# Kernel tuning notes

Hardware: AMD Instinct MI355X
Metric: run time of the kernel (lower is better)

Reference implementation:

```python
import jax, jax.numpy as jnp
import numpy as np

N = 4096; B = 32; LATENT = 16; UNITS = 64; NNZ = 65536; K = 2; M = 2 * K + 1

def _spmm(rows, cols, vals, x):
    # sparse [N,N] @ dense [N,FB] via gather + segment_sum
    return jax.ops.segment_sum(vals[:, None] * x[cols], rows, num_segments=N)

def _gconv(y, supports, W, b):
    # y: (B, N*F) -> Chebyshev-style diffusion over each support, then dense projection
    F = y.shape[1] // N
    x0 = y.reshape(B, N, F).transpose(1, 2, 0).reshape(N, F * B)
    xs = [x0]
    for rows, cols, vals in supports:
        x1 = _spmm(rows, cols, vals, x0)
        xs.append(x1)
        xk1, xk2 = x1, x0
        for _ in range(2, K + 1):
            x2 = 2.0 * _spmm(rows, cols, vals, xk1) - xk2
            xs.append(x2)
            xk1, xk2 = x2, xk1
    # [M,N,F,B] -> [B,N,F,M] -> [B*N, F*M], matching torch permute/reshape
    x = jnp.stack(xs).reshape(M, N, F, B).transpose(3, 1, 2, 0).reshape(B * N, F * M)
    return (x @ W + b).reshape(B, N * W.shape[1])

def setup_inputs():
    key = jax.random.key(0)
    ks = jax.random.split(key, 8)
    r = jax.random.randint(ks[0], (NNZ,), 0, N)
    c = jax.random.randint(ks[1], (NNZ,), 0, N)
    v = jax.random.uniform(ks[2], (NNZ,)) + 0.1
    d_row = jax.ops.segment_sum(v, r, num_segments=N)
    d_col = jax.ops.segment_sum(v, c, num_segments=N)
    inv_row = jnp.where(d_row > 0, 1.0 / d_row, 0.0)
    inv_col = jnp.where(d_col > 0, 1.0 / d_col, 0.0)
    # support1 = (D_out^{-1} A)^T ; support2 = (D_in^{-1} A^T)^T  (COO triples)
    s1_rows, s1_cols, s1_vals = c, r, v * inv_row[r]
    s2_rows, s2_cols, s2_vals = r, c, v * inv_col[c]
    def xavier(k, shape):
        scale = np.sqrt(2.0 / (shape[0] + shape[1])).astype(np.float32)
        return jax.random.normal(k, shape, dtype=jnp.float32) * scale
    return {
        "t_local": 0,
        "y": jax.random.normal(ks[3], (B, N * LATENT), dtype=jnp.float32),
        "W_theta": xavier(ks[4], (LATENT * M, LATENT)),
        "b_lat": jnp.ones((LATENT,), jnp.float32),  # bias_start=1.0; shared (LayerParams keys biases by length)
        "W_hid": xavier(ks[5], (LATENT * M, UNITS)),
        "b_hid": jnp.zeros((UNITS,), jnp.float32),
        "W_out": xavier(ks[6], (UNITS * M, LATENT)),
        "s1_rows": s1_rows, "s1_cols": s1_cols, "s1_vals": s1_vals,
        "s2_rows": s2_rows, "s2_cols": s2_cols, "s2_vals": s2_vals,
    }

def reference(t_local, y, W_theta, b_lat, W_hid, b_hid, W_out,
              s1_rows, s1_cols, s1_vals, s2_rows, s2_cols, s2_vals):
    supports = [(s1_rows, s1_cols, s1_vals), (s2_rows, s2_cols, s2_vals)]
    theta = jax.nn.sigmoid(_gconv(y, supports, W_theta, b_lat))
    c = jnp.tanh(_gconv(y, supports, W_hid, b_hid))   # gen_layers = 1
    c = jnp.tanh(_gconv(c, supports, W_out, b_lat))   # shared bias of length latent_dim
    return -theta * c
```

## Files before the change

kernel.cpp:

```cpp
#include <hip/hip_runtime.h>
#include <stdint.h>

#define NN    4096
#define BB    32
#define NNZE  65536
#define WA    512
#define WD    512

typedef __attribute__((ext_vector_type(8))) short bf16x8;
typedef __attribute__((ext_vector_type(4))) float f32x4;

__device__ __forceinline__ float bf2f_lo(unsigned int u) {
    union { unsigned int x; float f; } c; c.x = u << 16; return c.f;
}
__device__ __forceinline__ float bf2f_hi(unsigned int u) {
    union { unsigned int x; float f; } c; c.x = u & 0xffff0000u; return c.f;
}
__device__ __forceinline__ float bf2f(unsigned int h) {
    union { unsigned int u; float f; } c; c.u = h << 16; return c.f;
}
__device__ __forceinline__ unsigned int f2bf(float f) {
    union { float ff; unsigned int u; } c; c.ff = f;
    return (c.u + 0x7fffu + ((c.u >> 16) & 1u)) >> 16;
}

__global__ void hist2_kernel(const int* __restrict__ r1, const int* __restrict__ r2,
                             int* __restrict__ cnt1, int* __restrict__ cnt2) {
    int e = blockIdx.x * blockDim.x + threadIdx.x;
    if (e < NNZE) atomicAdd(&cnt1[r1[e]], 1);
    else          atomicAdd(&cnt2[r2[e - NNZE]], 1);
}

__global__ void scan2_kernel(int* cur1, int* rp1, int* cur2, int* rp2) {
    int* cur = (blockIdx.x == 0) ? cur1 : cur2;
    int* rp  = (blockIdx.x == 0) ? rp1  : rp2;
    __shared__ int part[256];
    int t = threadIdx.x;
    int base = t * 16;
    int loc[16];
    int s = 0;
#pragma unroll
    for (int i = 0; i < 16; ++i) { loc[i] = s; s += cur[base + i]; }
    part[t] = s;
    __syncthreads();
    for (int off = 1; off < 256; off <<= 1) {
        int v = 0;
        if (t >= off) v = part[t - off];
        __syncthreads();
        part[t] += v;
        __syncthreads();
    }
    int excl = (t == 0) ? 0 : part[t - 1];
#pragma unroll
    for (int i = 0; i < 16; ++i) rp[base + i] = excl + loc[i];
    __syncthreads();
#pragma unroll
    for (int i = 0; i < 16; ++i) cur[base + i] = rp[base + i];
    if (t == 255) rp[4096] = part[255];
}

__global__ void scatter2_kernel(const int* __restrict__ r1, const int* __restrict__ c1, const float* __restrict__ v1,
                                const int* __restrict__ r2, const int* __restrict__ c2, const float* __restrict__ v2,
                                int* __restrict__ cur1, int* __restrict__ cur2,
                                int2* __restrict__ ep1, int2* __restrict__ ep2) {
    int e = blockIdx.x * blockDim.x + threadIdx.x;
    if (e < NNZE) {
        int pos = atomicAdd(&cur1[r1[e]], 1);
        ep1[pos] = make_int2(c1[e], __float_as_int(v1[e]));
    } else {
        int ee = e - NNZE;
        int pos = atomicAdd(&cur2[r2[ee]], 1);
        ep2[pos] = make_int2(c2[ee], __float_as_int(v2[ee]));
    }
}

__global__ void transA_kernel(const float* __restrict__ y, unsigned short* __restrict__ x0h) {
    int t = threadIdx.x, n = blockIdx.x;
    int b = t & 31, q = t >> 5;
    float4 y4 = *(const float4*)(y + (size_t)b * (NN * 16) + n * 16 + 4 * q);
    uint2 o;
    o.x = f2bf(y4.x) | (f2bf(y4.y) << 16);
    o.y = f2bf(y4.z) | (f2bf(y4.w) << 16);
    *(uint2*)(x0h + (size_t)n * WA + b * 16 + 4 * q) = o;
}

struct SpmmDesc {
    const unsigned short* in;
    const unsigned short* prev;
    float* outF;
    unsigned short* outH;
    const int* rp; const int2* ep;
    float alpha, beta;
};

__device__ __forceinline__ void gather_row_lds(const unsigned short* __restrict__ in,
                                               const int* __restrict__ rp, const int2* __restrict__ ep,
                                               int row, int t, int* scol, float* sval, float* acc) {
    int beg = rp[row], end = rp[row + 1];
    for (int i0 = beg; i0 < end; i0 += 64) {
        int nn = end - i0; if (nn > 64) nn = 64;
        __syncthreads();
        if (t < nn) { int2 e = ep[i0 + t]; scol[t] = e.x; sval[t] = __int_as_float(e.y); }
        __syncthreads();
#pragma unroll 4
        for (int j = 0; j < nn; ++j) {
            const uint4* xr = (const uint4*)(in + (size_t)scol[j] * WD);
            uint4 xv = xr[t];
            float v = sval[j];
            acc[0] += v * bf2f_lo(xv.x); acc[1] += v * bf2f_hi(xv.x);
            acc[2] += v * bf2f_lo(xv.y); acc[3] += v * bf2f_hi(xv.y);
            acc[4] += v * bf2f_lo(xv.z); acc[5] += v * bf2f_hi(xv.z);
            acc[6] += v * bf2f_lo(xv.w); acc[7] += v * bf2f_hi(xv.w);
        }
    }
}

__launch_bounds__(64)
__global__ void spmmD_kernel(SpmmDesc q0, SpmmDesc q1, SpmmDesc q2, SpmmDesc q3, int ninst) {
    __shared__ int scol[64];
    __shared__ float sval[64];
    int blk = blockIdx.x;
    int xcd = blk & 7;
    int idx = blk >> 3;
    int spx = 8 / ninst;
    int inst = xcd / spx;
    int sub  = xcd - inst * spx;
    int row  = sub * (NN / spx) + idx;
    SpmmDesc q = (inst == 0) ? q0 : (inst == 1) ? q1 : (inst == 2) ? q2 : q3;
    int t = threadIdx.x;
    float acc[8];
#pragma unroll
    for (int k = 0; k < 8; ++k) acc[k] = 0.f;
    gather_row_lds(q.in, q.rp, q.ep, row, t, scol, sval, acc);
    float r[8];
#pragma unroll
    for (int k = 0; k < 8; ++k) r[k] = q.alpha * acc[k];
    if (q.prev) {
        uint4 pv = ((const uint4*)(q.prev + (size_t)row * WD))[t];
        r[0] += q.beta * bf2f_lo(pv.x); r[1] += q.beta * bf2f_hi(pv.x);
        r[2] += q.beta * bf2f_lo(pv.y); r[3] += q.beta * bf2f_hi(pv.y);
        r[4] += q.beta * bf2f_lo(pv.z); r[5] += q.beta * bf2f_hi(pv.z);
        r[6] += q.beta * bf2f_lo(pv.w); r[7] += q.beta * bf2f_hi(pv.w);
    }
    if (q.outF) {
        float* po = q.outF + (size_t)row * WD + t * 8;
        *(float4*)(po)     = make_float4(r[0], r[1], r[2], r[3]);
        *(float4*)(po + 4) = make_float4(r[4], r[5], r[6], r[7]);
    } else {
        uint4 o;
        o.x = f2bf(r[0]) | (f2bf(r[1]) << 16);
        o.y = f2bf(r[2]) | (f2bf(r[3]) << 16);
        o.z = f2bf(r[4]) | (f2bf(r[5]) << 16);
        o.w = f2bf(r[6]) | (f2bf(r[7]) << 16);
        ((uint4*)(q.outH + (size_t)row * WD))[t] = o;
    }
}

__launch_bounds__(256)
__global__ void proj_fused(const unsigned short* __restrict__ xh,
                           const float* __restrict__ Wtheta, const float* __restrict__ Whid,
                           const float* __restrict__ b_hid, const float* __restrict__ Wout,
                           float* __restrict__ theta,
                           float* __restrict__ d0,
                           unsigned short* __restrict__ dd1, unsigned short* __restrict__ dd2,
                           unsigned short* __restrict__ dd3, unsigned short* __restrict__ dd4) {
    __shared__ __align__(16) unsigned short sWa[80 * 104];
    __shared__ __align__(16) unsigned short sWo[80 * 72];
    __shared__ __align__(16) unsigned short sC[4][32 * 72];
    int t = threadIdx.x;
    for (int i = t; i < 80 * 96; i += 256) {
        int col = i / 96, k = i - col * 96;
        int m = k >> 4, f = k & 15;
        float v = 0.f;
        if (m < 5) v = (col < 16) ? Wtheta[(f * 5 + m) * 16 + col]
                                  : Whid[(f * 5 + m) * 64 + (col - 16)];
        sWa[col * 104 + k] = (unsigned short)f2bf(v);
    }
    for (int i = t; i < 80 * 64; i += 256) {
        int col = i >> 6, k = i & 63;
        int m = col >> 4, up = col & 15;
        sWo[col * 72 + k] = (unsigned short)f2bf(Wout[(k * 5 + m) * 16 + up]);
    }
    __syncthreads();
    int lane = t & 63, w = t >> 6;
    int r = lane & 15, g = lane >> 4;
    bf16x8 wfa[5][3];
#pragma unroll
    for (int ct = 0; ct < 5; ++ct)
#pragma unroll
        for (int kt = 0; kt < 3; ++kt)
            wfa[ct][kt] = *(const bf16x8*)(sWa + (ct * 16 + r) * 104 + kt * 32 + g * 8);
    float bh[4];
#pragma unroll
    for (int ct = 0; ct < 4; ++ct) bh[ct] = b_hid[ct * 16 + r];
    unsigned short* myC = (unsigned short*)sC[w];

    for (int i = 0; i < 2; ++i) {
        int n = blockIdx.x * 8 + w * 2 + i;
        f32x4 acc[2][5];
#pragma unroll
        for (int bt = 0; bt < 2; ++bt)
#pragma unroll
            for (int ct = 0; ct < 5; ++ct)
                acc[bt][ct] = (f32x4){0.f, 0.f, 0.f, 0.f};
#pragma unroll
        for (int kt = 0; kt < 3; ++kt) {
            bf16x8 a[2];
            int m = kt * 2 + (g >> 1);
#pragma unroll
            for (int bt = 0; bt < 2; ++bt) {
                bf16x8 av = {0, 0, 0, 0, 0, 0, 0, 0};
                if (m < 5)
                    av = *(const bf16x8*)(xh + ((size_t)m * NN + n) * WA
                                          + (bt * 16 + r) * 16 + (g & 1) * 8);
                a[bt] = av;
            }
#pragma unroll
            for (int bt = 0; bt < 2; ++bt)
#pragma unroll
                for (int ct = 0; ct < 5; ++ct)
                    acc[bt][ct] = __builtin_amdgcn_mfma_f32_16x16x32_bf16(
                        a[bt], wfa[ct][kt], acc[bt][ct], 0, 0, 0);
        }
#pragma unroll
        for (int bt = 0; bt < 2; ++bt) {
#pragma unroll
            for (int reg = 0; reg < 4; ++reg) {
                int b = bt * 16 + g * 4 + reg;
                theta[(size_t)n * 512 + b * 16 + r] = acc[bt][0][reg];
            }
#pragma unroll
            for (int ct = 1; ct < 5; ++ct) {
                int u = (ct - 1) * 16 + r;
#pragma unroll
                for (int reg = 0; reg < 4; ++reg) {
                    int b = bt * 16 + g * 4 + reg;
                    myC[b * 72 + u] = (unsigned short)f2bf(tanhf(acc[bt][ct][reg] + bh[ct - 1]));
                }
            }
        }
        f32x4 acc2[2][5];
#pragma unroll
        for (int bt = 0; bt < 2; ++bt)
#pragma unroll
            for (int ct = 0; ct < 5; ++ct)
                acc2[bt][ct] = (f32x4){0.f, 0.f, 0.f, 0.f};
#pragma unroll
        for (int kt = 0; kt < 2; ++kt) {
            bf16x8 a2[2];
#pragma unroll
            for (int bt = 0; bt < 2; ++bt)
                a2[bt] = *(const bf16x8*)(myC + (bt * 16 + r) * 72 + kt * 32 + g * 8);
#pragma unroll
            for (int ct = 0; ct < 5; ++ct) {
                bf16x8 wo = *(const bf16x8*)(sWo + (ct * 16 + r) * 72 + kt * 32 + g * 8);
#pragma unroll
                for (int bt = 0; bt < 2; ++bt)
                    acc2[bt][ct] = __builtin_amdgcn_mfma_f32_16x16x32_bf16(
                        a2[bt], wo, acc2[bt][ct], 0, 0, 0);
            }
        }
#pragma unroll
        for (int bt = 0; bt < 2; ++bt) {
#pragma unroll
            for (int reg = 0; reg < 4; ++reg) {
                int b = bt * 16 + g * 4 + reg;
                d0[(size_t)n * WD + b * 16 + r] = acc2[bt][0][reg];
            }
#pragma unroll
            for (int ct = 1; ct < 5; ++ct) {
                unsigned short* dp = (ct == 1) ? dd1 : (ct == 2) ? dd2 : (ct == 3) ? dd3 : dd4;
#pragma unroll
                for (int reg = 0; reg < 4; ++reg) {
                    int b = bt * 16 + g * 4 + reg;
                    dp[(size_t)n * WD + b * 16 + r] = (unsigned short)f2bf(acc2[bt][ct][reg]);
                }
            }
        }
    }
}

__launch_bounds__(64)
__global__ void finalspmm_kernel(const unsigned short* __restrict__ g1, const unsigned short* __restrict__ g3,
                                 const int* __restrict__ rp1, const int2* __restrict__ ep1,
                                 const int* __restrict__ rp2, const int2* __restrict__ ep2,
                                 const float* __restrict__ theta, const float* __restrict__ d0,
                                 const unsigned short* __restrict__ dd2, const unsigned short* __restrict__ dd4,
                                 const float* __restrict__ b_lat, float* __restrict__ out) {
    __shared__ int scol[64];
    __shared__ float sval[64];
    int blk = blockIdx.x;
    int row = (blk & 7) * 512 + (blk >> 3);
    int t = threadIdx.x;
    float h[8];
#pragma unroll
    for (int k = 0; k < 8; ++k) h[k] = 0.f;
    gather_row_lds(g1, rp1, ep1, row, t, scol, sval, h);
    gather_row_lds(g3, rp2, ep2, row, t, scol, sval, h);
    size_t base = (size_t)row * WD + t * 8;
    float4 dA = *(const float4*)(d0 + base);
    float4 dB = *(const float4*)(d0 + base + 4);
    uint4 p2 = *(const uint4*)(dd2 + base);
    uint4 p4 = *(const uint4*)(dd4 + base);
    float4 tA = *(const float4*)(theta + base);
    float4 tB = *(const float4*)(theta + base + 4);
    float4 blA = *(const float4*)(b_lat + (t & 1) * 8);
    float4 blB = *(const float4*)(b_lat + (t & 1) * 8 + 4);
    float tot[8], th[8];
    tot[0] = dA.x - bf2f_lo(p2.x) - bf2f_lo(p4.x) + h[0] + blA.x;
    tot[1] = dA.y - bf2f_hi(p2.x) - bf2f_hi(p4.x) + h[1] + blA.y;
    tot[2] = dA.z - bf2f_lo(p2.y) - bf2f_lo(p4.y) + h[2] + blA.z;
    tot[3] = dA.w - bf2f_hi(p2.y) - bf2f_hi(p4.y) + h[3] + blA.w;
    tot[4] = dB.x - bf2f_lo(p2.z) - bf2f_lo(p4.z) + h[4] + blB.x;
    tot[5] = dB.y - bf2f_hi(p2.z) - bf2f_hi(p4.z) + h[5] + blB.y;
    tot[6] = dB.z - bf2f_lo(p2.w) - bf2f_lo(p4.w) + h[6] + blB.z;
    tot[7] = dB.w - bf2f_hi(p2.w) - bf2f_hi(p4.w) + h[7] + blB.w;
    th[0] = tA.x + blA.x; th[1] = tA.y + blA.y; th[2] = tA.z + blA.z; th[3] = tA.w + blA.w;
    th[4] = tB.x + blB.x; th[5] = tB.y + blB.y; th[6] = tB.z + blB.z; th[7] = tB.w + blB.w;
    float res[8];
#pragma unroll
    for (int j = 0; j < 8; ++j)
        res[j] = -(1.f / (1.f + expf(-th[j]))) * tanhf(tot[j]);
    float* po = out + ((size_t)(t >> 1) * NN + row) * 16 + (t & 1) * 8;
    *(float4*)(po)     = make_float4(res[0], res[1], res[2], res[3]);
    *(float4*)(po + 4) = make_float4(res[4], res[5], res[6], res[7]);
}

extern "C" void kernel_launch(void* const* d_in, const int* in_sizes, int n_in,
                              void* d_out, int out_size, void* d_ws, size_t ws_size,
                              hipStream_t stream) {
    const float* y      = (const float*)d_in[1];
    const float* Wtheta = (const float*)d_in[2];
    const float* b_lat  = (const float*)d_in[3];
    const float* Whid   = (const float*)d_in[4];
    const float* b_hid  = (const float*)d_in[5];
    const float* Wout   = (const float*)d_in[6];
    const int*   r1     = (const int*)d_in[7];
    const int*   c1     = (const int*)d_in[8];
    const float* v1     = (const float*)d_in[9];
    const int*   r2     = (const int*)d_in[10];
    const int*   c2     = (const int*)d_in[11];
    const float* v2     = (const float*)d_in[12];
    float* out = (float*)d_out;

    char* ws = (char*)d_ws;
    size_t off = 0;
    auto alloc = [&](size_t bytes) -> char* {
        char* p = ws + off;
        off += (bytes + 255) & ~(size_t)255;
        return p;
    };
    int*   rp1   = (int*)alloc(4097 * 4);
    int*   rp2   = (int*)alloc(4097 * 4);
    int*   cur1  = (int*)alloc(4096 * 4);
    int*   cur2  = (int*)alloc(4096 * 4);
    int2*  ep1   = (int2*)alloc((size_t)NNZE * 8);
    int2*  ep2   = (int2*)alloc((size_t)NNZE * 8);
    unsigned short* xh = (unsigned short*)alloc((size_t)5 * NN * WA * 2);
    float* theta = (float*)alloc((size_t)NN * 512 * 4);
    float* d0    = (float*)alloc((size_t)NN * WD * 4);
    unsigned short* dd1 = (unsigned short*)alloc((size_t)NN * WD * 2);
    unsigned short* dd2 = (unsigned short*)alloc((size_t)NN * WD * 2);
    unsigned short* dd3 = (unsigned short*)alloc((size_t)NN * WD * 2);
    unsigned short* dd4 = (unsigned short*)alloc((size_t)NN * WD * 2);
    unsigned short* g1  = (unsigned short*)alloc((size_t)NN * WD * 2);
    unsigned short* g3  = (unsigned short*)alloc((size_t)NN * WD * 2);
    if (off > ws_size) return;

    unsigned short* x0h = xh;
    unsigned short* x1h = xh + (size_t)1 * NN * WA;
    unsigned short* x2h = xh + (size_t)2 * NN * WA;
    unsigned short* x3h = xh + (size_t)3 * NN * WA;
    unsigned short* x4h = xh + (size_t)4 * NN * WA;

    hipMemsetAsync(cur1, 0, 2 * 4096 * 4, stream);
    hist2_kernel<<<2 * NNZE / 256, 256, 0, stream>>>(r1, r2, cur1, cur2);
    scan2_kernel<<<2, 256, 0, stream>>>(cur1, rp1, cur2, rp2);
    scatter2_kernel<<<2 * NNZE / 256, 256, 0, stream>>>(r1, c1, v1, r2, c2, v2,
                                                        cur1, cur2, ep1, ep2);

    transA_kernel<<<NN, 128, 0, stream>>>(y, x0h);
    {
        SpmmDesc a0 = { x0h, nullptr, nullptr, x1h, rp1, ep1, 1.f, 0.f };
        SpmmDesc a1 = { x0h, nullptr, nullptr, x3h, rp2, ep2, 1.f, 0.f };
        spmmD_kernel<<<2 * NN, 64, 0, stream>>>(a0, a1, a0, a1, 2);
    }
    {
        SpmmDesc a0 = { x1h, x0h, nullptr, x2h, rp1, ep1, 2.f, -1.f };
        SpmmDesc a1 = { x3h, x0h, nullptr, x4h, rp2, ep2, 2.f, -1.f };
        spmmD_kernel<<<2 * NN, 64, 0, stream>>>(a0, a1, a0, a1, 2);
    }

    proj_fused<<<NN / 8, 256, 0, stream>>>(xh, Wtheta, Whid, b_hid, Wout,
                                           theta, d0, dd1, dd2, dd3, dd4);

    {
        SpmmDesc a0 = { dd2, dd1, nullptr, g1, rp1, ep1, 2.f, 1.f };
        SpmmDesc a1 = { dd4, dd3, nullptr, g3, rp2, ep2, 2.f, 1.f };
        spmmD_kernel<<<2 * NN, 64, 0, stream>>>(a0, a1, a0, a1, 2);
    }
    finalspmm_kernel<<<NN, 64, 0, stream>>>(g1, g3, rp1, ep1, rp2, ep2,
                                            theta, d0, dd2, dd4, b_lat, out);
}
```

Baseline: 199.4 us.

## Use wave-per-row SpMM and fold Chebyshev recurrence into projection weights

```diff
diff --git a/kernel.cpp b/kernel.cpp
--- a/kernel.cpp
+++ b/kernel.cpp
@@ -84,6 +84,25 @@
     *(uint2*)(x0h + (size_t)n * WA + b * 16 + 4 * q) = o;
 }
 
+__device__ __forceinline__ void gather_wave(const unsigned short* __restrict__ in,
+                                            int beg, int end, const int2* __restrict__ ep,
+                                            int lane, int* scol, float* sval, float* acc) {
+    for (int i0 = beg; i0 < end; i0 += 64) {
+        if (i0 + lane < end) { int2 e = ep[i0 + lane]; scol[lane] = e.x; sval[lane] = __int_as_float(e.y); }
+        int nn = end - i0; if (nn > 64) nn = 64;
+#pragma unroll 4
+        for (int j = 0; j < nn; ++j) {
+            const uint4* xr = (const uint4*)(in + (size_t)scol[j] * WD);
+            uint4 xv = xr[lane];
+            float v = sval[j];
+            acc[0] += v * bf2f_lo(xv.x); acc[1] += v * bf2f_hi(xv.x);
+            acc[2] += v * bf2f_lo(xv.y); acc[3] += v * bf2f_hi(xv.y);
+            acc[4] += v * bf2f_lo(xv.z); acc[5] += v * bf2f_hi(xv.z);
+            acc[6] += v * bf2f_lo(xv.w); acc[7] += v * bf2f_hi(xv.w);
+        }
+    }
+}
+
 struct SpmmDesc {
     const unsigned short* in;
     const unsigned short* prev;
@@ -93,57 +112,35 @@
     float alpha, beta;
 };
 
-__device__ __forceinline__ void gather_row_lds(const unsigned short* __restrict__ in,
-                                               const int* __restrict__ rp, const int2* __restrict__ ep,
-                                               int row, int t, int* scol, float* sval, float* acc) {
-    int beg = rp[row], end = rp[row + 1];
-    for (int i0 = beg; i0 < end; i0 += 64) {
-        int nn = end - i0; if (nn > 64) nn = 64;
-        __syncthreads();
-        if (t < nn) { int2 e = ep[i0 + t]; scol[t] = e.x; sval[t] = __int_as_float(e.y); }
-        __syncthreads();
-#pragma unroll 4
-        for (int j = 0; j < nn; ++j) {
-            const uint4* xr = (const uint4*)(in + (size_t)scol[j] * WD);
-            uint4 xv = xr[t];
-            float v = sval[j];
-            acc[0] += v * bf2f_lo(xv.x); acc[1] += v * bf2f_hi(xv.x);
-            acc[2] += v * bf2f_lo(xv.y); acc[3] += v * bf2f_hi(xv.y);
-            acc[4] += v * bf2f_lo(xv.z); acc[5] += v * bf2f_hi(xv.z);
-            acc[6] += v * bf2f_lo(xv.w); acc[7] += v * bf2f_hi(xv.w);
-        }
-    }
-}
-
-__launch_bounds__(64)
+__launch_bounds__(256)
 __global__ void spmmD_kernel(SpmmDesc q0, SpmmDesc q1, SpmmDesc q2, SpmmDesc q3, int ninst) {
-    __shared__ int scol[64];
-    __shared__ float sval[64];
+    __shared__ int  sscol[4][64];
+    __shared__ float ssval[4][64];
+    int t = threadIdx.x, w = t >> 6, lane = t & 63;
     int blk = blockIdx.x;
-    int xcd = blk & 7;
-    int idx = blk >> 3;
+    int xcd = blk & 7, idx = blk >> 3;
     int spx = 8 / ninst;
     int inst = xcd / spx;
     int sub  = xcd - inst * spx;
-    int row  = sub * (NN / spx) + idx;
+    int row  = sub * (NN / spx) + idx * 4 + w;
     SpmmDesc q = (inst == 0) ? q0 : (inst == 1) ? q1 : (inst == 2) ? q2 : q3;
-    int t = threadIdx.x;
+    int beg = q.rp[row], end = q.rp[row + 1];
     float acc[8];
 #pragma unroll
     for (int k = 0; k < 8; ++k) acc[k] = 0.f;
-    gather_row_lds(q.in, q.rp, q.ep, row, t, scol, sval, acc);
+    gather_wave(q.in, beg, end, q.ep, lane, sscol[w], ssval[w], acc);
     float r[8];
 #pragma unroll
     for (int k = 0; k < 8; ++k) r[k] = q.alpha * acc[k];
     if (q.prev) {
-        uint4 pv = ((const uint4*)(q.prev + (size_t)row * WD))[t];
+        uint4 pv = ((const uint4*)(q.prev + (size_t)row * WD))[lane];
         r[0] += q.beta * bf2f_lo(pv.x); r[1] += q.beta * bf2f_hi(pv.x);
         r[2] += q.beta * bf2f_lo(pv.y); r[3] += q.beta * bf2f_hi(pv.y);
         r[4] += q.beta * bf2f_lo(pv.z); r[5] += q.beta * bf2f_hi(pv.z);
         r[6] += q.beta * bf2f_lo(pv.w); r[7] += q.beta * bf2f_hi(pv.w);
     }
     if (q.outF) {
-        float* po = q.outF + (size_t)row * WD + t * 8;
+        float* po = q.outF + (size_t)row * WD + lane * 8;
         *(float4*)(po)     = make_float4(r[0], r[1], r[2], r[3]);
         *(float4*)(po + 4) = make_float4(r[4], r[5], r[6], r[7]);
     } else {
@@ -152,7 +149,7 @@
         o.y = f2bf(r[2]) | (f2bf(r[3]) << 16);
         o.z = f2bf(r[4]) | (f2bf(r[5]) << 16);
         o.w = f2bf(r[6]) | (f2bf(r[7]) << 16);
-        ((uint4*)(q.outH + (size_t)row * WD))[t] = o;
+        ((uint4*)(q.outH + (size_t)row * WD))[lane] = o;
     }
 }
 
@@ -172,8 +169,24 @@
         int col = i / 96, k = i - col * 96;
         int m = k >> 4, f = k & 15;
         float v = 0.f;
-        if (m < 5) v = (col < 16) ? Wtheta[(f * 5 + m) * 16 + col]
-                                  : Whid[(f * 5 + m) * 64 + (col - 16)];
+        if (m < 5) {
+            float w0, w2, w4, wm;
+            if (col < 16) {
+                w0 = Wtheta[(f * 5 + 0) * 16 + col];
+                w2 = Wtheta[(f * 5 + 2) * 16 + col];
+                w4 = Wtheta[(f * 5 + 4) * 16 + col];
+                wm = Wtheta[(f * 5 + m) * 16 + col];
+            } else {
+                w0 = Whid[(f * 5 + 0) * 64 + (col - 16)];
+                w2 = Whid[(f * 5 + 2) * 64 + (col - 16)];
+                w4 = Whid[(f * 5 + 4) * 64 + (col - 16)];
+                wm = Whid[(f * 5 + m) * 64 + (col - 16)];
+            }
+            if (m == 0) v = w0 - w2 - w4;
+            else if (m == 2) v = 2.f * w2;
+            else if (m == 4) v = 2.f * w4;
+            else v = wm;
+        }
         sWa[col * 104 + k] = (unsigned short)f2bf(v);
     }
     for (int i = t; i < 80 * 64; i += 256) {
@@ -195,117 +208,115 @@
     for (int ct = 0; ct < 4; ++ct) bh[ct] = b_hid[ct * 16 + r];
     unsigned short* myC = (unsigned short*)sC[w];
 
-    for (int i = 0; i < 2; ++i) {
-        int n = blockIdx.x * 8 + w * 2 + i;
-        f32x4 acc[2][5];
+    int n = blockIdx.x * 4 + w;
+    f32x4 acc[2][5];
+#pragma unroll
+    for (int bt = 0; bt < 2; ++bt)
+#pragma unroll
+        for (int ct = 0; ct < 5; ++ct)
+            acc[bt][ct] = (f32x4){0.f, 0.f, 0.f, 0.f};
+#pragma unroll
+    for (int kt = 0; kt < 3; ++kt) {
+        bf16x8 a[2];
+        int m = kt * 2 + (g >> 1);
+#pragma unroll
+        for (int bt = 0; bt < 2; ++bt) {
+            bf16x8 av = {0, 0, 0, 0, 0, 0, 0, 0};
+            if (m < 5)
+                av = *(const bf16x8*)(xh + ((size_t)m * NN + n) * WA
+                                      + (bt * 16 + r) * 16 + (g & 1) * 8);
+            a[bt] = av;
+        }
 #pragma unroll
         for (int bt = 0; bt < 2; ++bt)
 #pragma unroll
             for (int ct = 0; ct < 5; ++ct)
-                acc[bt][ct] = (f32x4){0.f, 0.f, 0.f, 0.f};
-#pragma unroll
-        for (int kt = 0; kt < 3; ++kt) {
-            bf16x8 a[2];
-            int m = kt * 2 + (g >> 1);
-#pragma unroll
-            for (int bt = 0; bt < 2; ++bt) {
-                bf16x8 av = {0, 0, 0, 0, 0, 0, 0, 0};
-                if (m < 5)
-                    av = *(const bf16x8*)(xh + ((size_t)m * NN + n) * WA
-                                          + (bt * 16 + r) * 16 + (g & 1) * 8);
-                a[bt] = av;
-            }
-#pragma unroll
-            for (int bt = 0; bt < 2; ++bt)
-#pragma unroll
-                for (int ct = 0; ct < 5; ++ct)
-                    acc[bt][ct] = __builtin_amdgcn_mfma_f32_16x16x32_bf16(
-                        a[bt], wfa[ct][kt], acc[bt][ct], 0, 0, 0);
-        }
-#pragma unroll
-        for (int bt = 0; bt < 2; ++bt) {
+                acc[bt][ct] = __builtin_amdgcn_mfma_f32_16x16x32_bf16(
+                    a[bt], wfa[ct][kt], acc[bt][ct], 0, 0, 0);
+    }
+#pragma unroll
+    for (int bt = 0; bt < 2; ++bt) {
+#pragma unroll
+        for (int reg = 0; reg < 4; ++reg) {
+            int b = bt * 16 + g * 4 + reg;
+            theta[(size_t)n * 512 + b * 16 + r] = acc[bt][0][reg];
+        }
+#pragma unroll
+        for (int ct = 1; ct < 5; ++ct) {
+            int u = (ct - 1) * 16 + r;
 #pragma unroll
             for (int reg = 0; reg < 4; ++reg) {
                 int b = bt * 16 + g * 4 + reg;
-                theta[(size_t)n * 512 + b * 16 + r] = acc[bt][0][reg];
+                myC[b * 72 + u] = (unsigned short)f2bf(tanhf(acc[bt][ct][reg] + bh[ct - 1]));
             }
-#pragma unroll
-            for (int ct = 1; ct < 5; ++ct) {
-                int u = (ct - 1) * 16 + r;
-#pragma unroll
-                for (int reg = 0; reg < 4; ++reg) {
-                    int b = bt * 16 + g * 4 + reg;
-                    myC[b * 72 + u] = (unsigned short)f2bf(tanhf(acc[bt][ct][reg] + bh[ct - 1]));
-                }
-            }
-        }
-        f32x4 acc2[2][5];
+        }
+    }
+    f32x4 acc2[2][5];
+#pragma unroll
+    for (int bt = 0; bt < 2; ++bt)
+#pragma unroll
+        for (int ct = 0; ct < 5; ++ct)
+            acc2[bt][ct] = (f32x4){0.f, 0.f, 0.f, 0.f};
+#pragma unroll
+    for (int kt = 0; kt < 2; ++kt) {
+        bf16x8 a2[2];
 #pragma unroll
         for (int bt = 0; bt < 2; ++bt)
-#pragma unroll
-            for (int ct = 0; ct < 5; ++ct)
-                acc2[bt][ct] = (f32x4){0.f, 0.f, 0.f, 0.f};
-#pragma unroll
-        for (int kt = 0; kt < 2; ++kt) {
-            bf16x8 a2[2];
+            a2[bt] = *(const bf16x8*)(myC + (bt * 16 + r) * 72 + kt * 32 + g * 8);
+#pragma unroll
+        for (int ct = 0; ct < 5; ++ct) {
+            bf16x8 wo = *(const bf16x8*)(sWo + (ct * 16 + r) * 72 + kt * 32 + g * 8);
 #pragma unroll
             for (int bt = 0; bt < 2; ++bt)
-                a2[bt] = *(const bf16x8*)(myC + (bt * 16 + r) * 72 + kt * 32 + g * 8);
-#pragma unroll
-            for (int ct = 0; ct < 5; ++ct) {
-                bf16x8 wo = *(const bf16x8*)(sWo + (ct * 16 + r) * 72 + kt * 32 + g * 8);
-#pragma unroll
-                for (int bt = 0; bt < 2; ++bt)
-                    acc2[bt][ct] = __builtin_amdgcn_mfma_f32_16x16x32_bf16(
-                        a2[bt], wo, acc2[bt][ct], 0, 0, 0);
-            }
-        }
-#pragma unroll
-        for (int bt = 0; bt < 2; ++bt) {
+                acc2[bt][ct] = __builtin_amdgcn_mfma_f32_16x16x32_bf16(
+                    a2[bt], wo, acc2[bt][ct], 0, 0, 0);
+        }
+    }
+#pragma unroll
+    for (int bt = 0; bt < 2; ++bt) {
+#pragma unroll
+        for (int reg = 0; reg < 4; ++reg) {
+            int b = bt * 16 + g * 4 + reg;
+            d0[(size_t)n * WD + b * 16 + r] = acc2[bt][0][reg];
+        }
+#pragma unroll
+        for (int ct = 1; ct < 5; ++ct) {
+            unsigned short* dp = (ct == 1) ? dd1 : (ct == 2) ? dd2 : (ct == 3) ? dd3 : dd4;
 #pragma unroll
             for (int reg = 0; reg < 4; ++reg) {
                 int b = bt * 16 + g * 4 + reg;
-                d0[(size_t)n * WD + b * 16 + r] = acc2[bt][0][reg];
+                dp[(size_t)n * WD + b * 16 + r] = (unsigned short)f2bf(acc2[bt][ct][reg]);
             }
-#pragma unroll
-            for (int ct = 1; ct < 5; ++ct) {
-                unsigned short* dp = (ct == 1) ? dd1 : (ct == 2) ? dd2 : (ct == 3) ? dd3 : dd4;
-#pragma unroll
-                for (int reg = 0; reg < 4; ++reg) {
-                    int b = bt * 16 + g * 4 + reg;
-                    dp[(size_t)n * WD + b * 16 + r] = (unsigned short)f2bf(acc2[bt][ct][reg]);
-                }
-            }
-        }
-    }
-}
-
-__launch_bounds__(64)
+        }
+    }
+}
+
+__launch_bounds__(256)
 __global__ void finalspmm_kernel(const unsigned short* __restrict__ g1, const unsigned short* __restrict__ g3,
                                  const int* __restrict__ rp1, const int2* __restrict__ ep1,
                                  const int* __restrict__ rp2, const int2* __restrict__ ep2,
                                  const float* __restrict__ theta, const float* __restrict__ d0,
                                  const unsigned short* __restrict__ dd2, const unsigned short* __restrict__ dd4,
                                  const float* __restrict__ b_lat, float* __restrict__ out) {
-    __shared__ int scol[64];
-    __shared__ float sval[64];
+    __shared__ int  sscol[4][64];
+    __shared__ float ssval[4][64];
+    int t = threadIdx.x, w = t >> 6, lane = t & 63;
     int blk = blockIdx.x;
-    int row = (blk & 7) * 512 + (blk >> 3);
-    int t = threadIdx.x;
+    int row = (blk & 7) * 512 + (blk >> 3) * 4 + w;
     float h[8];
 #pragma unroll
     for (int k = 0; k < 8; ++k) h[k] = 0.f;
-    gather_row_lds(g1, rp1, ep1, row, t, scol, sval, h);
-    gather_row_lds(g3, rp2, ep2, row, t, scol, sval, h);
-    size_t base = (size_t)row * WD + t * 8;
+    gather_wave(g1, rp1[row], rp1[row + 1], ep1, lane, sscol[w], ssval[w], h);
+    gather_wave(g3, rp2[row], rp2[row + 1], ep2, lane, sscol[w], ssval[w], h);
+    size_t base = (size_t)row * WD + lane * 8;
     float4 dA = *(const float4*)(d0 + base);
     float4 dB = *(const float4*)(d0 + base + 4);
     uint4 p2 = *(const uint4*)(dd2 + base);
     uint4 p4 = *(const uint4*)(dd4 + base);
     float4 tA = *(const float4*)(theta + base);
     float4 tB = *(const float4*)(theta + base + 4);
-    float4 blA = *(const float4*)(b_lat + (t & 1) * 8);
-    float4 blB = *(const float4*)(b_lat + (t & 1) * 8 + 4);
+    float4 blA = *(const float4*)(b_lat + (lane & 1) * 8);
+    float4 blB = *(const float4*)(b_lat + (lane & 1) * 8 + 4);
     float tot[8], th[8];
     tot[0] = dA.x - bf2f_lo(p2.x) - bf2f_lo(p4.x) + h[0] + blA.x;
     tot[1] = dA.y - bf2f_hi(p2.x) - bf2f_hi(p4.x) + h[1] + blA.y;
@@ -321,7 +332,7 @@
 #pragma unroll
     for (int j = 0; j < 8; ++j)
         res[j] = -(1.f / (1.f + expf(-th[j]))) * tanhf(tot[j]);
-    float* po = out + ((size_t)(t >> 1) * NN + row) * 16 + (t & 1) * 8;
+    float* po = out + ((size_t)(lane >> 1) * NN + row) * 16 + (lane & 1) * 8;
     *(float4*)(po)     = make_float4(res[0], res[1], res[2], res[3]);
     *(float4*)(po + 4) = make_float4(res[4], res[5], res[6], res[7]);
 }
@@ -383,22 +394,22 @@
     {
         SpmmDesc a0 = { x0h, nullptr, nullptr, x1h, rp1, ep1, 1.f, 0.f };
         SpmmDesc a1 = { x0h, nullptr, nullptr, x3h, rp2, ep2, 1.f, 0.f };
-        spmmD_kernel<<<2 * NN, 64, 0, stream>>>(a0, a1, a0, a1, 2);
+        spmmD_kernel<<<2 * NN / 4, 256, 0, stream>>>(a0, a1, a0, a1, 2);
     }
     {
-        SpmmDesc a0 = { x1h, x0h, nullptr, x2h, rp1, ep1, 2.f, -1.f };
-        SpmmDesc a1 = { x3h, x0h, nullptr, x4h, rp2, ep2, 2.f, -1.f };
-        spmmD_kernel<<<2 * NN, 64, 0, stream>>>(a0, a1, a0, a1, 2);
-    }
-
-    proj_fused<<<NN / 8, 256, 0, stream>>>(xh, Wtheta, Whid, b_hid, Wout,
+        SpmmDesc a0 = { x1h, nullptr, nullptr, x2h, rp1, ep1, 1.f, 0.f };
+        SpmmDesc a1 = { x3h, nullptr, nullptr, x4h, rp2, ep2, 1.f, 0.f };
+        spmmD_kernel<<<2 * NN / 4, 256, 0, stream>>>(a0, a1, a0, a1, 2);
+    }
+
+    proj_fused<<<NN / 4, 256, 0, stream>>>(xh, Wtheta, Whid, b_hid, Wout,
                                            theta, d0, dd1, dd2, dd3, dd4);
 
     {
         SpmmDesc a0 = { dd2, dd1, nullptr, g1, rp1, ep1, 2.f, 1.f };
         SpmmDesc a1 = { dd4, dd3, nullptr, g3, rp2, ep2, 2.f, 1.f };
-        spmmD_kernel<<<2 * NN, 64, 0, stream>>>(a0, a1, a0, a1, 2);
-    }
-    finalspmm_kernel<<<NN, 64, 0, stream>>>(g1, g3, rp1, ep1, rp2, ep2,
-                                            theta, d0, dd2, dd4, b_lat, out);
-}
+        spmmD_kernel<<<2 * NN / 4, 256, 0, stream>>>(a0, a1, a0, a1, 2);
+    }
+    finalspmm_kernel<<<NN / 4, 256, 0, stream>>>(g1, g3, rp1, ep1, rp2, ep2,
+                                                 theta, d0, dd2, dd4, b_lat, out);
+}
```

New measurement: 232.4 us. 1.17x slower.
